# Kernel tuning notes

Hardware: AMD Instinct MI355X
Metric: run time of the kernel (lower is better)

The kernel has to match this reference:

```python
import jax, jax.numpy as jnp
import numpy as np

DIM = 1024
NUM_PATTERNS = 8192
B, S = 2, 4096


def setup_inputs() -> dict:
    key = jax.random.key(0)
    k1, k2, k3 = jax.random.split(key, 3)
    scale = 1.0 / np.sqrt(DIM)
    x = jax.random.normal(k1, (B, S, DIM), dtype=jnp.float32)
    # nn.Linear default init ~ U(-1/sqrt(in), 1/sqrt(in)); normal*scale is fine for a baseline
    w_q = jax.random.normal(k2, (DIM, DIM), dtype=jnp.float32) * scale
    xi = jax.random.normal(k3, (NUM_PATTERNS, DIM), dtype=jnp.float32) * scale
    beta = jnp.float32(1.0 / np.sqrt(DIM))
    return {"x": x, "w_q": w_q, "xi": xi, "beta": beta}


def reference(x, w_q, xi, beta):
    # q = x @ w_q.T  (torch F.linear convention: weight is [out, in])
    q = jnp.einsum("bsd,ed->bse", x, w_q)
    # logits = beta * q @ xi.T  -> [B, S, P]
    logits = beta * jnp.einsum("bsd,pd->bsp", q, xi)
    attn = jax.nn.softmax(logits, axis=-1)
    # retrieve patterns: attn @ xi -> [B, S, dim]
    return jnp.einsum("bsp,pd->bsd", attn, xi)
```

## Files before the change

### kernel.cpp

```cpp
#include <hip/hip_runtime.h>


typedef __attribute__((ext_vector_type(8))) int int8v;
typedef __attribute__((ext_vector_type(4))) float f32x4;

#define NDIM 1024
#define NPAT 8192
#define NROW 8192

__device__ __forceinline__ unsigned f8pack4(float a, float b, float c, float d) {
  int w = __builtin_amdgcn_cvt_pk_fp8_f32(a, b, 0, false);
  w = __builtin_amdgcn_cvt_pk_fp8_f32(c, d, w, true);
  return (unsigned)w;
}
__device__ __forceinline__ unsigned char f8b(float v) {
  return (unsigned char)(__builtin_amdgcn_cvt_pk_fp8_f32(v, v, 0, false) & 0xff);
}
__device__ __forceinline__ int sig(int c) {
  return (c & 64) | ((c & 15) << 2) | ((c >> 4) & 3);
}

__device__ __forceinline__ void gload_lds16(const void* g, void* l) {
  __builtin_amdgcn_global_load_lds(
      (const __attribute__((address_space(1))) unsigned char*)g,
      (__attribute__((address_space(3))) unsigned char*)l,
      16, 0, 0);
}


__global__ void cast_f8(const float* __restrict__ in,
                        unsigned* __restrict__ out, float scale, int n4) {
  int i = blockIdx.x * blockDim.x + threadIdx.x;
  if (i < n4) {
    float4 v = ((const float4*)in)[i];
    out[i] = f8pack4(v.x * scale, v.y * scale, v.z * scale, v.w * scale);
  }
}

__global__ void xi_prep8(const float* __restrict__ xi,
                         unsigned char* __restrict__ xi8,
                         unsigned char* __restrict__ xit8,
                         float* __restrict__ colsum) {
  __shared__ float t[32][33];
  __shared__ float cs[8][32];
  int tx = threadIdx.x, ty = threadIdx.y;
  int d0 = blockIdx.x * 32, p0 = blockIdx.y * 32;
  int d = d0 + tx;
  int di = (d & ~127) + sig(d & 127);
  float psum = 0.f;
#pragma unroll
  for (int j = 0; j < 32; j += 8) {
    float v = xi[(long)(p0 + ty + j) * NDIM + d];
    t[ty + j][tx] = v;
    psum += v;
    xi8[(long)(p0 + ty + j) * NDIM + di] = f8b(32.f * v);
  }
  cs[ty][tx] = psum;
  __syncthreads();
  if (ty == 0) {
    float s = 0.f;
#pragma unroll
    for (int k = 0; k < 8; ++k) s += cs[k][tx];
    atomicAdd(&colsum[d0 + tx], s);
  }
  int p = p0 + tx;
  int pi = (p & ~127) + sig(p & 127);
#pragma unroll
  for (int j = 0; j < 32; j += 8)
    xit8[(long)(d0 + ty + j) * NPAT + pi] = f8b(32.f * t[tx][ty + j]);
}


template <int MODE>
__launch_bounds__(256, 2)
__global__ void gemm_f8(const unsigned char* __restrict__ A,
                        const unsigned char* __restrict__ B,
                        void* __restrict__ Cv, int N, int K,
                        const float* __restrict__ beta_ptr,
                        const float* __restrict__ rowsum,
                        const float* __restrict__ colsum,
                        float* __restrict__ rowsum_out) {
  __shared__ unsigned char smem[32768];
  char* Asm = (char*)smem;
  char* Bsm = (char*)smem + 16384;

  const int tid = threadIdx.x;
  const int wave = tid >> 6;
  const int lane = tid & 63;
  const int wm = wave >> 1, wn = wave & 1;
  const int quad = lane >> 4, ln = lane & 15;

  const long row0 = (long)blockIdx.y * 128;
  const long col0 = (long)blockIdx.x * 128;

  const int r_in = lane >> 3;
  const int csl = lane & 7;
  const int cg = ((((csl >> 1) ^ (r_in & 3)) << 1) | (csl & 1));
  const unsigned char* gA[4];
  const unsigned char* gB[4];
  char* lA[4];
  char* lB[4];
#pragma unroll
  for (int p = 0; p < 4; ++p) {
    int grp = wave * 4 + p;
    gA[p] = A + (row0 + grp * 8 + r_in) * (long)K + cg * 16;
    gB[p] = B + (col0 + grp * 8 + r_in) * (long)K + cg * 16;
    lA[p] = Asm + grp * 1024;
    lB[p] = Bsm + grp * 1024;
  }

  const int ps = (quad ^ (ln & 3)) * 32;
  const int base_a = (wm * 64 + ln) * 128 + ps;
  const int base_b = (wn * 64 + ln) * 128 + ps;

  f32x4 acc[4][4] = {};

  for (int kt = 0; kt < K; kt += 128) {
#pragma unroll
    for (int p = 0; p < 4; ++p) gload_lds16(gA[p], lA[p]);
#pragma unroll
    for (int p = 0; p < 4; ++p) gload_lds16(gB[p], lB[p]);
#pragma unroll
    for (int p = 0; p < 4; ++p) { gA[p] += 128; gB[p] += 128; }
    __syncthreads();

    int8v af[4], bfv[4];
#pragma unroll
    for (int t = 0; t < 4; ++t)
      af[t] = *(const int8v*)(Asm + base_a + t * 2048);
#pragma unroll
    for (int t = 0; t < 4; ++t)
      bfv[t] = *(const int8v*)(Bsm + base_b + t * 2048);
#pragma unroll
    for (int mt = 0; mt < 4; ++mt)
#pragma unroll
      for (int nt = 0; nt < 4; ++nt)
        acc[mt][nt] = __builtin_amdgcn_mfma_scale_f32_16x16x128_f8f6f4(
            af[mt], bfv[nt], acc[mt][nt], 0, 0, 0, 0x7f7f7f7f, 0, 0x7f7f7f7f);
    __syncthreads();
  }

  if (MODE == 0) {
    unsigned* C32 = (unsigned*)Cv;
    const float s = 1.0f / 32.0f;
#pragma unroll
    for (int mt = 0; mt < 4; ++mt)
#pragma unroll
      for (int r = 0; r < 4; ++r) {
        long row = row0 + wm * 64 + mt * 16 + quad * 4 + r;
        unsigned w = f8pack4(acc[mt][0][r] * s, acc[mt][1][r] * s,
                             acc[mt][2][r] * s, acc[mt][3][r] * s);
        C32[row * (N >> 2) + (col0 >> 2) + wn * 16 + ln] = w;
      }
  } else if (MODE == 1) {
    unsigned* C32 = (unsigned*)Cv;
    const float bs = beta_ptr[0] * (1.0f / 32.0f);
#pragma unroll
    for (int mt = 0; mt < 4; ++mt)
#pragma unroll
      for (int r = 0; r < 4; ++r) {
        long row = row0 + wm * 64 + mt * 16 + quad * 4 + r;
        float e0 = (__expf(bs * acc[mt][0][r]) - 1.0f) * 32.f;
        float e1 = (__expf(bs * acc[mt][1][r]) - 1.0f) * 32.f;
        float e2 = (__expf(bs * acc[mt][2][r]) - 1.0f) * 32.f;
        float e3 = (__expf(bs * acc[mt][3][r]) - 1.0f) * 32.f;
        C32[row * (N >> 2) + (col0 >> 2) + wn * 16 + ln] =
            f8pack4(e0, e1, e2, e3);
        float s = e0 + e1 + e2 + e3;
        s += __shfl_xor(s, 1, 64);
        s += __shfl_xor(s, 2, 64);
        s += __shfl_xor(s, 4, 64);
        s += __shfl_xor(s, 8, 64);
        if (ln == 0) atomicAdd(&rowsum_out[row], s);
      }
  } else {
    float* C = (float*)Cv;
#pragma unroll
    for (int mt = 0; mt < 4; ++mt)
#pragma unroll
      for (int r = 0; r < 4; ++r) {
        long row = row0 + wm * 64 + mt * 16 + quad * 4 + r;
        float inv = 1.0f / (8192.0f + rowsum[row] * (1.0f / 32.0f));
#pragma unroll
        for (int nt = 0; nt < 4; ++nt) {
          long col = col0 + wn * 64 + nt * 16 + ln;
          C[row * N + col] =
              (acc[mt][nt][r] * (1.0f / 1024.0f) + colsum[col]) * inv;
        }
      }
  }
}


extern "C" void kernel_launch(void* const* d_in, const int* in_sizes, int n_in,
                              void* d_out, int out_size, void* d_ws,
                              size_t ws_size, hipStream_t stream) {
  const float* x    = (const float*)d_in[0];
  const float* wq   = (const float*)d_in[1];
  const float* xi   = (const float*)d_in[2];
  const float* beta = (const float*)d_in[3];
  float* out = (float*)d_out;

  char* ws = (char*)d_ws;
  const size_t MB = 1024 * 1024;
  unsigned char* x8   = (unsigned char*)(ws);
  unsigned char* wq8  = (unsigned char*)(ws + 8 * MB);
  unsigned char* q8   = (unsigned char*)(ws + 9 * MB);
  unsigned char* xi8  = (unsigned char*)(ws + 17 * MB);
  unsigned char* xit8 = (unsigned char*)(ws + 25 * MB);
  float*         rs   = (float*)(ws + 33 * MB);
  float*         csum = (float*)(ws + 33 * MB + 32768);
  unsigned char* E8   = (unsigned char*)(ws + 34 * MB);

  hipMemsetAsync(rs, 0, 36864, stream);

  cast_f8<<<(NROW * NDIM / 4) / 256, 256, 0, stream>>>(
      x, (unsigned*)x8, 1.0f, NROW * NDIM / 4);
  cast_f8<<<(NDIM * NDIM / 4) / 256, 256, 0, stream>>>(
      wq, (unsigned*)wq8, 32.0f, NDIM * NDIM / 4);
  xi_prep8<<<dim3(NDIM / 32, NPAT / 32), dim3(32, 8), 0, stream>>>(
      xi, xi8, xit8, csum);

  gemm_f8<0><<<dim3(NDIM / 128, NROW / 128), 256, 0, stream>>>(
      x8, wq8, q8, NDIM, NDIM, nullptr, nullptr, nullptr, nullptr);

  gemm_f8<1><<<dim3(NPAT / 128, NROW / 128), 256, 0, stream>>>(
      q8, xi8, E8, NPAT, NDIM, beta, nullptr, nullptr, rs);

  gemm_f8<2><<<dim3(NDIM / 128, NROW / 128), 256, 0, stream>>>(
      E8, xit8, out, NDIM, NPAT, nullptr, rs, csum, nullptr);
}
```

Before: 334.4 us.

## Rewrite FP8 GEMM with double-buffered LDS pipeline, larger tiles and XCD remap

Replaces the single-buffered 128x128 FP8 GEMM with a 512-thread kernel using 128/256x256 tiles and double-buffered LDS. Async global-to-LDS loads for the next k-tiles are split into four phases interleaved with MFMA work, using explicit barriers, waitcnt and setprio. Block indices are remapped across chiplets to improve L2 locality, and LDS reads use a new XOR swizzle. The aim is to hide global load latency and raise MFMA utilisation, at the cost of more LDS and register pressure plus fragile manual synchronisation.

New measurement: 399.9 us. 1.2x slower.

```diff
diff --git a/kernel.cpp b/kernel.cpp
--- a/kernel.cpp
+++ b/kernel.cpp
@@ -1,6 +1,7 @@
 #include <hip/hip_runtime.h>
 
 
+typedef __attribute__((ext_vector_type(4))) int int4v;
 typedef __attribute__((ext_vector_type(8))) int int8v;
 typedef __attribute__((ext_vector_type(4))) float f32x4;
 
@@ -71,99 +72,158 @@
 }
 
 
-template <int MODE>
-__launch_bounds__(256, 2)
-__global__ void gemm_f8(const unsigned char* __restrict__ A,
-                        const unsigned char* __restrict__ B,
-                        void* __restrict__ Cv, int N, int K,
-                        const float* __restrict__ beta_ptr,
-                        const float* __restrict__ rowsum,
-                        const float* __restrict__ colsum,
-                        float* __restrict__ rowsum_out) {
-  __shared__ unsigned char smem[32768];
-  char* Asm = (char*)smem;
-  char* Bsm = (char*)smem + 16384;
+#define STAGE_A(MQ, T, BO)                                                  \
+  _Pragma("unroll") for (int R = 0; R < aR; ++R)                            \
+      gload_lds16(pA[MQ][R] + ((long)(T) << 7), dA[MQ][R] + (BO));
+
+#define STAGE_B(NQ, T, BO)                                                  \
+  _Pragma("unroll") for (int R = 0; R < 2; ++R)                             \
+      gload_lds16(pB[NQ][R] + ((long)(T) << 7), dB[NQ][R] + (BO));
+
+#define PHASE(MQ, NQ, STAGE_STMT, DO_VM)                                    \
+  {                                                                         \
+    const unsigned char* sb = smem + bo;                                    \
+    int8v af[MH], bf[2];                                                    \
+    _Pragma("unroll") for (int t = 0; t < MH; ++t) {                        \
+      int off = arow + ((MQ) * MH + t) * 2048;                              \
+      int4v lo = *(const int4v*)(sb + off + sxr);                           \
+      int4v hi = *(const int4v*)(sb + off + sxr1);                          \
+      af[t] = __builtin_shufflevector(lo, hi, 0, 1, 2, 3, 4, 5, 6, 7);      \
+    }                                                                       \
+    _Pragma("unroll") for (int u = 0; u < 2; ++u) {                         \
+      int off = brow + ((NQ) * 2 + u) * 2048;                               \
+      int4v lo = *(const int4v*)(sb + off + sxr);                           \
+      int4v hi = *(const int4v*)(sb + off + sxr1);                          \
+      bf[u] = __builtin_shufflevector(lo, hi, 0, 1, 2, 3, 4, 5, 6, 7);      \
+    }                                                                       \
+    STAGE_STMT;                                                             \
+    __builtin_amdgcn_s_barrier();                                           \
+    asm volatile("s_waitcnt lgkmcnt(0)" ::: "memory");                      \
+    __builtin_amdgcn_sched_barrier(0);                                      \
+    __builtin_amdgcn_s_setprio(1);                                          \
+    _Pragma("unroll") for (int mt = 0; mt < MH; ++mt)                       \
+      _Pragma("unroll") for (int nt = 0; nt < 2; ++nt)                      \
+        acc[(MQ) * MH + mt][(NQ) * 2 + nt] =                                \
+            __builtin_amdgcn_mfma_scale_f32_16x16x128_f8f6f4(               \
+                af[mt], bf[nt], acc[(MQ) * MH + mt][(NQ) * 2 + nt], 0, 0,   \
+                0, 0x7f7f7f7f, 0, 0x7f7f7f7f);                              \
+    __builtin_amdgcn_s_setprio(0);                                          \
+    if (DO_VM) asm volatile("s_waitcnt vmcnt(%0)" ::"n"(VM) : "memory");    \
+    __builtin_amdgcn_s_barrier();                                           \
+    __builtin_amdgcn_sched_barrier(0);                                      \
+  }
+
+template <int MODE, int BM>
+__launch_bounds__(512, 2)
+__global__ void gemm8(const unsigned char* __restrict__ A,
+                      const unsigned char* __restrict__ B,
+                      void* __restrict__ Cv, int N, int K,
+                      const float* __restrict__ beta_ptr,
+                      const float* __restrict__ rowsum,
+                      const float* __restrict__ colsum,
+                      float* __restrict__ rowsum_out) {
+  constexpr int MF = BM / 32;
+  constexpr int MH = MF / 2;
+  constexpr int MH16 = MH * 16;
+  constexpr int aR = BM / 128;
+  constexpr int VM = aR + 2;
+  constexpr int ABYTES = BM * 128;
+  constexpr int BUF = ABYTES + 32768;
+
+  __shared__ unsigned char smem[2 * BUF];
 
   const int tid = threadIdx.x;
-  const int wave = tid >> 6;
   const int lane = tid & 63;
-  const int wm = wave >> 1, wn = wave & 1;
+  const int wm = (tid >> 6) >> 2;
+  const int wn = (tid >> 6) & 3;
   const int quad = lane >> 4, ln = lane & 15;
 
-  const long row0 = (long)blockIdx.y * 128;
-  const long col0 = (long)blockIdx.x * 128;
-
-  const int r_in = lane >> 3;
-  const int csl = lane & 7;
-  const int cg = ((((csl >> 1) ^ (r_in & 3)) << 1) | (csl & 1));
-  const unsigned char* gA[4];
-  const unsigned char* gB[4];
-  char* lA[4];
-  char* lB[4];
-#pragma unroll
-  for (int p = 0; p < 4; ++p) {
-    int grp = wave * 4 + p;
-    gA[p] = A + (row0 + grp * 8 + r_in) * (long)K + cg * 16;
-    gB[p] = B + (col0 + grp * 8 + r_in) * (long)K + cg * 16;
-    lA[p] = Asm + grp * 1024;
-    lB[p] = Bsm + grp * 1024;
-  }
-
-  const int ps = (quad ^ (ln & 3)) * 32;
-  const int base_a = (wm * 64 + ln) * 128 + ps;
-  const int base_b = (wn * 64 + ln) * 128 + ps;
-
-  f32x4 acc[4][4] = {};
-
-  for (int kt = 0; kt < K; kt += 128) {
-#pragma unroll
-    for (int p = 0; p < 4; ++p) gload_lds16(gA[p], lA[p]);
-#pragma unroll
-    for (int p = 0; p < 4; ++p) gload_lds16(gB[p], lB[p]);
-#pragma unroll
-    for (int p = 0; p < 4; ++p) { gA[p] += 128; gB[p] += 128; }
-    __syncthreads();
-
-    int8v af[4], bfv[4];
-#pragma unroll
-    for (int t = 0; t < 4; ++t)
-      af[t] = *(const int8v*)(Asm + base_a + t * 2048);
-#pragma unroll
-    for (int t = 0; t < 4; ++t)
-      bfv[t] = *(const int8v*)(Bsm + base_b + t * 2048);
-#pragma unroll
-    for (int mt = 0; mt < 4; ++mt)
-#pragma unroll
-      for (int nt = 0; nt < 4; ++nt)
-        acc[mt][nt] = __builtin_amdgcn_mfma_scale_f32_16x16x128_f8f6f4(
-            af[mt], bfv[nt], acc[mt][nt], 0, 0, 0, 0x7f7f7f7f, 0, 0x7f7f7f7f);
-    __syncthreads();
-  }
+  const int nwg = gridDim.x;
+  int wg = blockIdx.x;
+  wg = (wg & 7) * (nwg >> 3) + (wg >> 3);
+  const int nbx = N >> 8;
+  const long row0 = (long)(wg / nbx) * BM;
+  const long col0 = (long)(wg % nbx) * 256;
+  const int nkt = K >> 7;
+
+  const int sx = (((tid & 7) ^ ((tid >> 3) & 7)) << 4);
+  const int jt = tid >> 3;
+  const int j0 = (tid >> 6) << 3;
+
+  const unsigned char* pA[2][aR]; unsigned char* dA[2][aR];
+  const unsigned char* pB[2][2];  unsigned char* dB[2][2];
+#pragma unroll
+  for (int q = 0; q < 2; ++q) {
+#pragma unroll
+    for (int R = 0; R < aR; ++R) {
+      int j = R * 64 + jt;
+      int r = q * MH16 + (j % MH16) + (j / MH16) * (BM / 2);
+      int jr0 = R * 64 + j0;
+      int r0 = q * MH16 + (jr0 % MH16) + (jr0 / MH16) * (BM / 2);
+      pA[q][R] = A + (row0 + r) * (long)K + sx;
+      dA[q][R] = smem + r0 * 128;
+    }
+#pragma unroll
+    for (int R = 0; R < 2; ++R) {
+      int j = R * 64 + jt;
+      int r = q * 32 + (j & 31) + (j >> 5) * 64;
+      int jr0 = R * 64 + j0;
+      int r0 = q * 32 + (jr0 & 31) + (jr0 >> 5) * 64;
+      pB[q][R] = B + (col0 + r) * (long)K + sx;
+      dB[q][R] = smem + ABYTES + r0 * 128;
+    }
+  }
+
+  const int sxr = (((2 * quad) ^ (ln & 7)) << 4);
+  const int sxr1 = sxr ^ 16;
+  const int arow = (wm * (BM / 2) + ln) * 128;
+  const int brow = ABYTES + (wn * 64 + ln) * 128;
+
+  f32x4 acc[MF][4] = {};
+
+  STAGE_A(0, 0, 0); STAGE_B(0, 0, 0); STAGE_A(1, 0, 0); STAGE_B(1, 0, 0);
+  STAGE_A(0, 1, BUF); STAGE_B(0, 1, BUF);
+  asm volatile("s_waitcnt vmcnt(%0)" ::"n"(VM) : "memory");
+  __builtin_amdgcn_s_barrier();
+  __builtin_amdgcn_sched_barrier(0);
+
+#pragma unroll 2
+  for (int i = 0; i < nkt; ++i) {
+    const int bo = (i & 1) * BUF;
+    const int nbo = BUF - bo;
+    const int t1 = (i + 1 < nkt) ? i + 1 : nkt - 1;
+    const int t2 = (i + 2 < nkt) ? i + 2 : nkt - 1;
+    PHASE(0, 0, STAGE_A(1, t1, nbo), false);
+    PHASE(0, 1, STAGE_B(1, t1, nbo), false);
+    PHASE(1, 0, STAGE_A(0, t2, bo), false);
+    PHASE(1, 1, STAGE_B(0, t2, bo), true);
+  }
+  asm volatile("s_waitcnt vmcnt(0)" ::: "memory");
 
   if (MODE == 0) {
     unsigned* C32 = (unsigned*)Cv;
     const float s = 1.0f / 32.0f;
 #pragma unroll
-    for (int mt = 0; mt < 4; ++mt)
+    for (int mf = 0; mf < MF; ++mf)
 #pragma unroll
       for (int r = 0; r < 4; ++r) {
-        long row = row0 + wm * 64 + mt * 16 + quad * 4 + r;
-        unsigned w = f8pack4(acc[mt][0][r] * s, acc[mt][1][r] * s,
-                             acc[mt][2][r] * s, acc[mt][3][r] * s);
+        long row = row0 + wm * (BM / 2) + mf * 16 + quad * 4 + r;
+        unsigned w = f8pack4(acc[mf][0][r] * s, acc[mf][1][r] * s,
+                             acc[mf][2][r] * s, acc[mf][3][r] * s);
         C32[row * (N >> 2) + (col0 >> 2) + wn * 16 + ln] = w;
       }
   } else if (MODE == 1) {
     unsigned* C32 = (unsigned*)Cv;
     const float bs = beta_ptr[0] * (1.0f / 32.0f);
 #pragma unroll
-    for (int mt = 0; mt < 4; ++mt)
+    for (int mf = 0; mf < MF; ++mf)
 #pragma unroll
       for (int r = 0; r < 4; ++r) {
-        long row = row0 + wm * 64 + mt * 16 + quad * 4 + r;
-        float e0 = (__expf(bs * acc[mt][0][r]) - 1.0f) * 32.f;
-        float e1 = (__expf(bs * acc[mt][1][r]) - 1.0f) * 32.f;
-        float e2 = (__expf(bs * acc[mt][2][r]) - 1.0f) * 32.f;
-        float e3 = (__expf(bs * acc[mt][3][r]) - 1.0f) * 32.f;
+        long row = row0 + wm * (BM / 2) + mf * 16 + quad * 4 + r;
+        float e0 = (__expf(bs * acc[mf][0][r]) - 1.0f) * 32.f;
+        float e1 = (__expf(bs * acc[mf][1][r]) - 1.0f) * 32.f;
+        float e2 = (__expf(bs * acc[mf][2][r]) - 1.0f) * 32.f;
+        float e3 = (__expf(bs * acc[mf][3][r]) - 1.0f) * 32.f;
         C32[row * (N >> 2) + (col0 >> 2) + wn * 16 + ln] =
             f8pack4(e0, e1, e2, e3);
         float s = e0 + e1 + e2 + e3;
@@ -176,16 +236,16 @@
   } else {
     float* C = (float*)Cv;
 #pragma unroll
-    for (int mt = 0; mt < 4; ++mt)
+    for (int mf = 0; mf < MF; ++mf)
 #pragma unroll
       for (int r = 0; r < 4; ++r) {
-        long row = row0 + wm * 64 + mt * 16 + quad * 4 + r;
+        long row = row0 + wm * (BM / 2) + mf * 16 + quad * 4 + r;
         float inv = 1.0f / (8192.0f + rowsum[row] * (1.0f / 32.0f));
 #pragma unroll
-        for (int nt = 0; nt < 4; ++nt) {
-          long col = col0 + wn * 64 + nt * 16 + ln;
+        for (int nf = 0; nf < 4; ++nf) {
+          long col = col0 + wn * 64 + nf * 16 + ln;
           C[row * N + col] =
-              (acc[mt][nt][r] * (1.0f / 1024.0f) + colsum[col]) * inv;
+              (acc[mf][nf][r] * (1.0f / 1024.0f) + colsum[col]) * inv;
         }
       }
   }
@@ -221,12 +281,12 @@
   xi_prep8<<<dim3(NDIM / 32, NPAT / 32), dim3(32, 8), 0, stream>>>(
       xi, xi8, xit8, csum);
 
-  gemm_f8<0><<<dim3(NDIM / 128, NROW / 128), 256, 0, stream>>>(
+  gemm8<0, 128><<<(NROW / 128) * (NDIM / 256), 512, 0, stream>>>(
       x8, wq8, q8, NDIM, NDIM, nullptr, nullptr, nullptr, nullptr);
 
-  gemm_f8<1><<<dim3(NPAT / 128, NROW / 128), 256, 0, stream>>>(
+  gemm8<1, 256><<<(NROW / 256) * (NPAT / 256), 512, 0, stream>>>(
       q8, xi8, E8, NPAT, NDIM, beta, nullptr, nullptr, rs);
 
-  gemm_f8<2><<<dim3(NDIM / 128, NROW / 128), 256, 0, stream>>>(
+  gemm8<2, 128><<<(NROW / 128) * (NDIM / 256), 512, 0, stream>>>(
       E8, xit8, out, NDIM, NPAT, nullptr, rs, csum, nullptr);
 }
```

## Double-buffer LDS tiles in the fp8 GEMM and raise MFMA wave priority

Applied to the files above, without the earlier changes.

Shared memory grows to two 32KB stages, so the global-to-LDS load for the next K tile is issued before the MFMAs on the current tile run. This removes the first of the two barriers per iteration and is meant to hide global load latency behind compute. The MFMA block is also wrapped in s_setprio to favour waves doing math. The larger LDS footprint per block could limit how many blocks fit on a CU.

Result: slower. 360.5 us (+7.8%).

```diff
diff --git a/kernel.cpp b/kernel.cpp
--- a/kernel.cpp
+++ b/kernel.cpp
@@ -80,9 +80,7 @@
                         const float* __restrict__ rowsum,
                         const float* __restrict__ colsum,
                         float* __restrict__ rowsum_out) {
-  __shared__ unsigned char smem[32768];
-  char* Asm = (char*)smem;
-  char* Bsm = (char*)smem + 16384;
+  __shared__ unsigned char smem[65536];
 
   const int tid = threadIdx.x;
   const int wave = tid >> 6;
@@ -98,45 +96,61 @@
   const int cg = ((((csl >> 1) ^ (r_in & 3)) << 1) | (csl & 1));
   const unsigned char* gA[4];
   const unsigned char* gB[4];
-  char* lA[4];
-  char* lB[4];
+  int lA[4], lB[4];
 #pragma unroll
   for (int p = 0; p < 4; ++p) {
     int grp = wave * 4 + p;
     gA[p] = A + (row0 + grp * 8 + r_in) * (long)K + cg * 16;
     gB[p] = B + (col0 + grp * 8 + r_in) * (long)K + cg * 16;
-    lA[p] = Asm + grp * 1024;
-    lB[p] = Bsm + grp * 1024;
+    lA[p] = grp * 1024;
+    lB[p] = 16384 + grp * 1024;
   }
 
   const int ps = (quad ^ (ln & 3)) * 32;
   const int base_a = (wm * 64 + ln) * 128 + ps;
-  const int base_b = (wn * 64 + ln) * 128 + ps;
+  const int base_b = 16384 + (wn * 64 + ln) * 128 + ps;
 
   f32x4 acc[4][4] = {};
-
-  for (int kt = 0; kt < K; kt += 128) {
-#pragma unroll
-    for (int p = 0; p < 4; ++p) gload_lds16(gA[p], lA[p]);
-#pragma unroll
-    for (int p = 0; p < 4; ++p) gload_lds16(gB[p], lB[p]);
-#pragma unroll
-    for (int p = 0; p < 4; ++p) { gA[p] += 128; gB[p] += 128; }
-    __syncthreads();
+  const int nkt = K >> 7;
+
+#pragma unroll
+  for (int p = 0; p < 4; ++p) gload_lds16(gA[p], smem + lA[p]);
+#pragma unroll
+  for (int p = 0; p < 4; ++p) gload_lds16(gB[p], smem + lB[p]);
+#pragma unroll
+  for (int p = 0; p < 4; ++p) { gA[p] += 128; gB[p] += 128; }
+  __syncthreads();
+
+#pragma unroll 2
+  for (int kt = 0; kt < nkt; ++kt) {
+    const unsigned char* sb = smem + (kt & 1) * 32768;
+    unsigned char* sn = smem + ((kt + 1) & 1) * 32768;
+
+    if (kt + 1 < nkt) {
+#pragma unroll
+      for (int p = 0; p < 4; ++p) gload_lds16(gA[p], sn + lA[p]);
+#pragma unroll
+      for (int p = 0; p < 4; ++p) gload_lds16(gB[p], sn + lB[p]);
+#pragma unroll
+      for (int p = 0; p < 4; ++p) { gA[p] += 128; gB[p] += 128; }
+    }
 
     int8v af[4], bfv[4];
 #pragma unroll
     for (int t = 0; t < 4; ++t)
-      af[t] = *(const int8v*)(Asm + base_a + t * 2048);
+      af[t] = *(const int8v*)(sb + base_a + t * 2048);
 #pragma unroll
     for (int t = 0; t < 4; ++t)
-      bfv[t] = *(const int8v*)(Bsm + base_b + t * 2048);
+      bfv[t] = *(const int8v*)(sb + base_b + t * 2048);
+    __builtin_amdgcn_s_setprio(1);
 #pragma unroll
     for (int mt = 0; mt < 4; ++mt)
 #pragma unroll
       for (int nt = 0; nt < 4; ++nt)
         acc[mt][nt] = __builtin_amdgcn_mfma_scale_f32_16x16x128_f8f6f4(
             af[mt], bfv[nt], acc[mt][nt], 0, 0, 0, 0x7f7f7f7f, 0, 0x7f7f7f7f);
+    __builtin_amdgcn_s_setprio(0);
+
     __syncthreads();
   }
 
```

## Load B fragments directly to registers with double-buffered prefetch, keep A in LDS

Applied to the files above, without the earlier changes.

The GEMM kernel no longer stages the B tile through shared memory. Each wave reads its B fragments straight from global memory into registers, one K-step ahead, using two ping-pong register sets. Only A still goes through LDS, which halves the LDS footprint, and MFMA blocks are wrapped in s_setprio raises. The aim is to hide B load latency and cut LDS traffic. The cost is that B is fetched twice, once by each wave row, and A loads are still not overlapped, since they remain serialized between two barriers.

Result: slower. 479.6 us (+43.4%).

```diff
diff --git a/kernel.cpp b/kernel.cpp
--- a/kernel.cpp
+++ b/kernel.cpp
@@ -71,6 +71,29 @@
 }
 
 
+#define KITER(BF_CUR, BF_NXT, KT)                                           \
+  {                                                                         \
+    const long ob = (long)((KT) + 1 < nkt ? (KT) + 1 : nkt - 1) << 7;       \
+    _Pragma("unroll") for (int nt = 0; nt < 4; ++nt)                        \
+        BF_NXT[nt] = *(const int8v*)(pBf[nt] + ob);                         \
+    int8v af[4];                                                            \
+    _Pragma("unroll") for (int t = 0; t < 4; ++t)                           \
+        af[t] = *(const int8v*)(smem + base_a + t * 2048);                  \
+    __builtin_amdgcn_s_setprio(1);                                          \
+    _Pragma("unroll") for (int mt = 0; mt < 4; ++mt)                        \
+      _Pragma("unroll") for (int nt = 0; nt < 4; ++nt)                      \
+        acc[mt][nt] = __builtin_amdgcn_mfma_scale_f32_16x16x128_f8f6f4(     \
+            af[mt], BF_CUR[nt], acc[mt][nt], 0, 0, 0, 0x7f7f7f7f, 0,        \
+            0x7f7f7f7f);                                                    \
+    __builtin_amdgcn_s_setprio(0);                                          \
+    __syncthreads();                                                        \
+    if ((KT) + 1 < nkt) {                                                   \
+      _Pragma("unroll") for (int p = 0; p < 4; ++p)                         \
+          gload_lds16(gA[p] + (((long)(KT) + 1) << 7), lA[p]);              \
+    }                                                                       \
+    __syncthreads();                                                        \
+  }
+
 template <int MODE>
 __launch_bounds__(256, 2)
 __global__ void gemm_f8(const unsigned char* __restrict__ A,
@@ -80,9 +103,7 @@
                         const float* __restrict__ rowsum,
                         const float* __restrict__ colsum,
                         float* __restrict__ rowsum_out) {
-  __shared__ unsigned char smem[32768];
-  char* Asm = (char*)smem;
-  char* Bsm = (char*)smem + 16384;
+  __shared__ unsigned char smem[16384];
 
   const int tid = threadIdx.x;
   const int wave = tid >> 6;
@@ -97,47 +118,35 @@
   const int csl = lane & 7;
   const int cg = ((((csl >> 1) ^ (r_in & 3)) << 1) | (csl & 1));
   const unsigned char* gA[4];
-  const unsigned char* gB[4];
-  char* lA[4];
-  char* lB[4];
+  unsigned char* lA[4];
 #pragma unroll
   for (int p = 0; p < 4; ++p) {
     int grp = wave * 4 + p;
     gA[p] = A + (row0 + grp * 8 + r_in) * (long)K + cg * 16;
-    gB[p] = B + (col0 + grp * 8 + r_in) * (long)K + cg * 16;
-    lA[p] = Asm + grp * 1024;
-    lB[p] = Bsm + grp * 1024;
+    lA[p] = smem + grp * 1024;
   }
 
   const int ps = (quad ^ (ln & 3)) * 32;
   const int base_a = (wm * 64 + ln) * 128 + ps;
-  const int base_b = (wn * 64 + ln) * 128 + ps;
+
+  const unsigned char* pBf[4];
+#pragma unroll
+  for (int nt = 0; nt < 4; ++nt)
+    pBf[nt] = B + (col0 + wn * 64 + nt * 16 + ln) * (long)K + quad * 32;
 
   f32x4 acc[4][4] = {};
-
-  for (int kt = 0; kt < K; kt += 128) {
-#pragma unroll
-    for (int p = 0; p < 4; ++p) gload_lds16(gA[p], lA[p]);
-#pragma unroll
-    for (int p = 0; p < 4; ++p) gload_lds16(gB[p], lB[p]);
-#pragma unroll
-    for (int p = 0; p < 4; ++p) { gA[p] += 128; gB[p] += 128; }
-    __syncthreads();
-
-    int8v af[4], bfv[4];
-#pragma unroll
-    for (int t = 0; t < 4; ++t)
-      af[t] = *(const int8v*)(Asm + base_a + t * 2048);
-#pragma unroll
-    for (int t = 0; t < 4; ++t)
-      bfv[t] = *(const int8v*)(Bsm + base_b + t * 2048);
-#pragma unroll
-    for (int mt = 0; mt < 4; ++mt)
-#pragma unroll
-      for (int nt = 0; nt < 4; ++nt)
-        acc[mt][nt] = __builtin_amdgcn_mfma_scale_f32_16x16x128_f8f6f4(
-            af[mt], bfv[nt], acc[mt][nt], 0, 0, 0, 0x7f7f7f7f, 0, 0x7f7f7f7f);
-    __syncthreads();
+  const int nkt = K >> 7;
+
+  int8v bf0[4], bf1[4];
+#pragma unroll
+  for (int nt = 0; nt < 4; ++nt) bf0[nt] = *(const int8v*)(pBf[nt]);
+#pragma unroll
+  for (int p = 0; p < 4; ++p) gload_lds16(gA[p], lA[p]);
+  __syncthreads();
+
+  for (int kt = 0; kt < nkt; kt += 2) {
+    KITER(bf0, bf1, kt)
+    KITER(bf1, bf0, kt + 1)
   }
 
   if (MODE == 0) {
```
